# Performance work log

Hardware: AMD Instinct MI355X
Metric: run time of the kernel (lower is better)

The kernel has to match this reference:

```python
import jax, jax.numpy as jnp
from jax import lax
import numpy as np

# --- module constants (from init_kwargs) ---
MAXK = 512
BLOCK = 3            # Shi-Tomasi structure-tensor window
NUM_PAIRS = 256      # BAD descriptor dimensionality
ITERS = 20           # Sinkhorn iterations
EPS = 1.0            # entropy regularization
UNUSED = 1.0         # dustbin score
NMS_R = 3
THR = 0.0
PATCH_R = 8          # BAD pair-offset radius
BOX = 5              # BAD pre-smoothing box size

# fixed BAD comparison-pair offsets (dy1,dx1,dy2,dx2) -- constants, not learned
_OFFSETS = jnp.asarray(
    np.random.RandomState(42).randint(-PATCH_R, PATCH_R + 1, size=(NUM_PAIRS, 4)),
    dtype=jnp.int32)

_SOBEL_X = jnp.array([[-1., 0., 1.], [-2., 0., 2.], [-1., 0., 1.]], jnp.float32)[None, None]
_SOBEL_Y = jnp.transpose(_SOBEL_X, (0, 1, 3, 2))


def _conv(x, k):  # x: [B,1,H,W], k: [1,1,kh,kw]
    return lax.conv_general_dilated(x, k, (1, 1), 'SAME',
                                    dimension_numbers=('NCHW', 'OIHW', 'NCHW'))


def _detector(img):
    """Shi-Tomasi min-eigenvalue score map + dense BAD descriptor map."""
    Ix = _conv(img, _SOBEL_X)
    Iy = _conv(img, _SOBEL_Y)
    box = jnp.ones((1, 1, BLOCK, BLOCK), jnp.float32) / (BLOCK * BLOCK)
    Ixx = _conv(Ix * Ix, box)
    Iyy = _conv(Iy * Iy, box)
    Ixy = _conv(Ix * Iy, box)
    score = 0.5 * ((Ixx + Iyy) - jnp.sqrt((Ixx - Iyy) ** 2 + 4.0 * Ixy ** 2 + 1e-12))

    smooth = _conv(img, jnp.ones((1, 1, BOX, BOX), jnp.float32) / (BOX * BOX))[:, 0]  # [B,H,W]
    B, H, W = smooth.shape
    pad = jnp.pad(smooth, ((0, 0), (PATCH_R, PATCH_R), (PATCH_R, PATCH_R)), mode='edge')

    def one_pair(off):  # box-average difference at two shifted locations
        a = lax.dynamic_slice(pad, (0, PATCH_R + off[0], PATCH_R + off[1]), (B, H, W))
        b = lax.dynamic_slice(pad, (0, PATCH_R + off[2], PATCH_R + off[3]), (B, H, W))
        return a - b

    desc = jax.vmap(one_pair)(_OFFSETS)           # [D,B,H,W]
    return score[:, 0], jnp.transpose(desc, (1, 0, 2, 3))  # [B,H,W], [B,D,H,W]


def _nms_topk(score):
    """Max-pool NMS + top-k keypoint selection; invalid kpts = (-1,-1)."""
    win = 2 * NMS_R + 1
    mx = lax.reduce_window(score, -jnp.inf, lax.max, (1, win, win), (1, 1, 1), 'SAME')
    mask = (score >= mx) & (score > THR)
    B, H, W = score.shape
    masked = jnp.where(mask, score, -jnp.inf).reshape(B, H * W)
    vals, idx = lax.top_k(masked, MAXK)
    valid = jnp.isfinite(vals)
    y = (idx // W).astype(jnp.float32)
    x = (idx % W).astype(jnp.float32)
    kpts = jnp.where(valid[..., None], jnp.stack([y, x], -1), -1.0)  # [B,K,2] (y,x)
    return kpts


def _extract(desc_map, kpts):
    """Bilinear (subpixel) descriptor gather; zeros for invalid keypoints."""
    B, D, H, W = desc_map.shape
    valid = (kpts[:, :, 0] >= 0).astype(desc_map.dtype)
    y = jnp.clip(kpts[:, :, 0], 0.0, H - 1.0)
    x = jnp.clip(kpts[:, :, 1], 0.0, W - 1.0)
    y0 = jnp.floor(y); x0 = jnp.floor(x)
    y1 = jnp.minimum(y0 + 1.0, H - 1.0); x1 = jnp.minimum(x0 + 1.0, W - 1.0)
    wy = y - y0; wx = x - x0
    y0i, y1i = y0.astype(jnp.int32), y1.astype(jnp.int32)
    x0i, x1i = x0.astype(jnp.int32), x1.astype(jnp.int32)
    flat = desc_map.reshape(B, D, H * W)

    def g(yi, xi):  # [B,K] -> [B,D,K]
        return jnp.take_along_axis(flat, (yi * W + xi)[:, None, :], axis=2)

    d = (g(y0i, x0i) * ((1 - wy) * (1 - wx))[:, None, :]
         + g(y0i, x1i) * ((1 - wy) * wx)[:, None, :]
         + g(y1i, x0i) * (wy * (1 - wx))[:, None, :]
         + g(y1i, x1i) * (wy * wx)[:, None, :])
    return jnp.transpose(d, (0, 2, 1)) * valid[..., None]  # [B,K,D]


def _sinkhorn(d1, d2):
    """Log-domain Sinkhorn with dustbin row/col (SuperGlue-style OT)."""
    s1 = jnp.sum(d1 * d1, -1)
    s2 = jnp.sum(d2 * d2, -1)
    dist = jnp.sqrt(jnp.clip(
        s1[:, :, None] + s2[:, None, :] - 2.0 * jnp.einsum('bkd,bld->bkl', d1, d2),
        1e-12))
    B, K, _ = dist.shape
    Z = jnp.full((B, K + 1, K + 1), UNUSED / EPS, dtype=dist.dtype)
    Z = Z.at[:, :K, :K].set(-dist / EPS)
    norm = -jnp.log(2.0 * K)
    log_mu = jnp.concatenate([jnp.zeros((K,), Z.dtype),
                              jnp.log(jnp.full((1,), float(K), Z.dtype))]) + norm
    log_nu = log_mu

    def body(_, uv):
        u, v = uv
        u = log_mu - jax.scipy.special.logsumexp(Z + v[:, None, :], axis=2)
        v = log_nu - jax.scipy.special.logsumexp(Z + u[:, :, None], axis=1)
        return (u, v)

    u0 = jnp.zeros((B, K + 1), Z.dtype)
    u, v = lax.fori_loop(0, ITERS, body, (u0, u0))
    return jnp.exp(Z + u[:, :, None] + v[:, None, :] - norm)  # [B,K+1,K+1]


def _l2norm(d):
    return d / (jnp.linalg.norm(d, axis=-1, keepdims=True) + 1e-12)


def setup_inputs() -> dict:
    key = jax.random.key(0)
    k1, k2 = jax.random.split(key)
    image1 = jax.random.uniform(k1, (1, 1, 480, 640), jnp.float32)
    image2 = jax.random.uniform(k2, (1, 1, 480, 640), jnp.float32)
    return {"image1": image1, "image2": image2}


def reference(image1, image2):
    s1, m1 = _detector(image1)
    s2, m2 = _detector(image2)
    kpts1 = _nms_topk(s1)
    kpts2 = _nms_topk(s2)
    d1 = _l2norm(_extract(m1, kpts1))
    d2 = _l2norm(_extract(m2, kpts2))
    probs = _sinkhorn(d1, d2)
    return (kpts1, kpts2, probs)
```

## Files before the change

### kernel.cpp

```cpp
#include <hip/hip_runtime.h>
#include <math.h>
#include <stdint.h>

#define HH 480
#define WW 640
#define HW (HH*WW)
#define KK 512
#define DD 256
#define KP1 513
#define NSLOT 16
#define NBX 40
#define NBY 30
#define SLOTS_PER_IMG (NBX*NBY*NSLOT)
#define SVN 1024
#define SB 32
#define NORM_F (-6.9314718055994531f)
#define LOGK_F (6.2383246250395077f)
#define MU0 (1.0f/1024.0f)
#define MU1 (0.5f)

#define OFF_SURV   0u
#define OFF_Z      16384u
#define OFF_SMOOTH 2473984u
#define OFF_CAND   4931584u
#define OFF_KIDX   5238784u
#define OFF_DESC   5242880u
#define OFF_SBUF   6291456u
#define OFF_PCA    6295552u
#define OFF_PCB    6361216u
#define OFF_VA     6426880u
#define OFF_VB     6429184u
#define OFF_U      6431488u
#define OFF_SVCNT  6438912u

struct OffsTab { int v[1024]; };
static constexpr OffsTab make_offsets() {
  OffsTab o{};
  unsigned st[624] = {};
  st[0] = 42u;
  for (int i = 1; i < 624; ++i)
    st[i] = 1812433253u*(st[i-1] ^ (st[i-1] >> 30)) + (unsigned)i;
  int idx = 624, got = 0;
  while (got < 1024) {
    if (idx == 624) {
      for (int i = 0; i < 624; ++i) {
        unsigned y = (st[i] & 0x80000000u) | (st[(i+1)%624] & 0x7fffffffu);
        st[i] = st[(i+397)%624] ^ (y >> 1) ^ ((y & 1u) ? 2567483615u : 0u);
      }
      idx = 0;
    }
    unsigned y = st[idx++];
    y ^= y >> 11;
    y ^= (y << 7)  & 2636928640u;
    y ^= (y << 15) & 4022730752u;
    y ^= y >> 18;
    unsigned mv = y & 31u;
    if (mv <= 16u) { o.v[got] = (int)mv - 8; ++got; }
  }
  return o;
}
__device__ __constant__ OffsTab OFFS = make_offsets();

__global__ __launch_bounds__(256) void detnms_kernel(const float* __restrict__ img0,
    const float* __restrict__ img1, float* __restrict__ smooth,
    unsigned long long* __restrict__ cand) {
  __shared__ float tile[26][26];
  __shared__ float ixA[24][24], iyA[24][24];
  __shared__ float sc[22][22];
  __shared__ float vs[16][26];
  __shared__ float vm[16][22];
  __shared__ int wsum[4], wbase[4];
  const int imgI = blockIdx.z;
  const float* img = imgI ? img1 : img0;
  const int bx0 = blockIdx.x*16, by0 = blockIdx.y*16;
  const int tx = threadIdx.x, ty = threadIdx.y, lt = ty*16+tx;
  for (int p = lt; p < 676; p += 256) {
    int r = p/26, c = p%26;
    int gy = by0-5+r, gx = bx0-5+c;
    tile[r][c] = (gy >= 0 && gy < HH && gx >= 0 && gx < WW) ? img[gy*WW+gx] : 0.f;
  }
  __syncthreads();
  for (int p = lt; p < 576; p += 256) {
    int r = p/24, c = p%24;
    int gy = by0-4+r, gx = bx0-4+c;
    float ix = 0.f, iy = 0.f;
    if (gy >= 0 && gy < HH && gx >= 0 && gx < WW) {
      float t00 = tile[r][c],   t01 = tile[r][c+1],   t02 = tile[r][c+2];
      float t10 = tile[r+1][c],                        t12 = tile[r+1][c+2];
      float t20 = tile[r+2][c], t21 = tile[r+2][c+1], t22 = tile[r+2][c+2];
      ix = t00*(-1.f) + t02*1.f + t10*(-2.f) + t12*2.f + t20*(-1.f) + t22*1.f;
      iy = t00*(-1.f) + t01*(-2.f) + t02*(-1.f) + t20*1.f + t21*2.f + t22*1.f;
    }
    ixA[r][c] = ix; iyA[r][c] = iy;
  }
  __syncthreads();
  const float c9 = 1.f/9.f, c25 = 1.f/25.f;
  for (int p = lt; p < 484; p += 256) {
    int r = p/22, c = p%22;
    int gy = by0-3+r, gx = bx0-3+c;
    float v = -INFINITY;
    if (gy >= 0 && gy < HH && gx >= 0 && gx < WW) {
      float sxx = 0.f, syy = 0.f, sxy = 0.f;
      for (int dr = 0; dr < 3; ++dr)
        for (int dc = 0; dc < 3; ++dc) {
          float jx = ixA[r+dr][c+dc], jy = iyA[r+dr][c+dc];
          float pxxv = jx*jx, pyyv = jy*jy, pxyv = jx*jy;
          sxx += pxxv*c9; syy += pyyv*c9; sxy += pxyv*c9;
        }
      float tdif = sxx - syy;
      v = 0.5f * ((sxx + syy) - sqrtf(tdif*tdif + 4.f*(sxy*sxy) + 1e-12f));
    }
    sc[r][c] = v;
  }
  for (int p = lt; p < 416; p += 256) {
    int i = p/26, c = p%26;
    vs[i][c] = tile[i+3][c] + tile[i+4][c] + tile[i+5][c] + tile[i+6][c] + tile[i+7][c];
  }
  __syncthreads();
  for (int p = lt; p < 352; p += 256) {
    int i = p/22, c = p%22;
    float m = sc[i][c];
    m = fmaxf(m, sc[i+1][c]); m = fmaxf(m, sc[i+2][c]); m = fmaxf(m, sc[i+3][c]);
    m = fmaxf(m, sc[i+4][c]); m = fmaxf(m, sc[i+5][c]); m = fmaxf(m, sc[i+6][c]);
    vm[i][c] = m;
  }
  float sm = (vs[ty][tx+3] + vs[ty][tx+4] + vs[ty][tx+5] + vs[ty][tx+6] + vs[ty][tx+7]) * c25;
  smooth[imgI*HW + (by0+ty)*WW + (bx0+tx)] = sm;
  __syncthreads();
  float cv = sc[ty+3][tx+3];
  float m = vm[ty][tx];
  m = fmaxf(m, vm[ty][tx+1]); m = fmaxf(m, vm[ty][tx+2]); m = fmaxf(m, vm[ty][tx+3]);
  m = fmaxf(m, vm[ty][tx+4]); m = fmaxf(m, vm[ty][tx+5]); m = fmaxf(m, vm[ty][tx+6]);
  bool pred = (cv >= m && cv > 0.f);
  unsigned long long mask = __ballot(pred);
  int lane = lt & 63, wid = lt >> 6;
  if (lane == 0) wsum[wid] = __popcll(mask);
  __syncthreads();
  if (lt == 0) {
    int s0 = wsum[0], s1 = wsum[1], s2 = wsum[2], s3 = wsum[3];
    wbase[0] = 0; wbase[1] = s0; wbase[2] = s0+s1; wbase[3] = s0+s1+s2;
    wsum[0] = s0+s1+s2+s3;
  }
  __syncthreads();
  const int total = wsum[0];
  const size_t slotBase = (size_t)imgI*SLOTS_PER_IMG + (size_t)(blockIdx.y*NBX + blockIdx.x)*NSLOT;
  if (pred) {
    int pos = wbase[wid] + __popcll(mask & ((1ull << lane) - 1ull));
    if (pos < NSLOT) {
      int idx = (by0+ty)*WW + (bx0+tx);
      unsigned int ub = __float_as_uint(cv) | 0x80000000u;
      cand[slotBase + pos] = ((unsigned long long)ub << 32) | (unsigned int)(~idx);
    }
  }
  if (lt >= total && lt < NSLOT) cand[slotBase + lt] = 0ull;
}

__global__ __launch_bounds__(1024) void select2a_kernel(const unsigned long long* __restrict__ cand,
    unsigned long long* __restrict__ surv, int* __restrict__ svcnt) {
  __shared__ int hist[1024];
  __shared__ int sB1, sB2, sNeed, sCount;
  const int imgI = blockIdx.x, t = threadIdx.x;
  const unsigned long long* cd = cand + (size_t)imgI*SLOTS_PER_IMG;
  unsigned long long kreg[19];
  #pragma unroll
  for (int r = 0; r < 19; ++r) {
    int i = t + r*1024;
    kreg[r] = (i < SLOTS_PER_IMG) ? cd[i] : 0ull;
  }
  hist[t] = 0;
  if (t == 0) { sB1 = -1; sB2 = 0; sCount = 0; }
  __syncthreads();
  #pragma unroll
  for (int r = 0; r < 19; ++r)
    if (kreg[r]) atomicAdd(&hist[(int)(kreg[r] >> 54)], 1);
  __syncthreads();
  for (int d = 1; d < 1024; d <<= 1) {
    int vv = hist[t] + ((t + d < 1024) ? hist[t + d] : 0);
    __syncthreads();
    hist[t] = vv;
    __syncthreads();
  }
  if (hist[t] >= KK) atomicMax(&sB1, t);
  __syncthreads();
  const int b1 = sB1;
  if (t == 0 && b1 >= 0) sNeed = KK - ((b1 < 1023) ? hist[b1 + 1] : 0);
  __syncthreads();
  int b2 = 0;
  if (b1 >= 0) {
    hist[t] = 0;
    __syncthreads();
    #pragma unroll
    for (int r = 0; r < 19; ++r) {
      unsigned long long k = kreg[r];
      if (k && (int)(k >> 54) == b1) atomicAdd(&hist[(int)(k >> 44) & 1023], 1);
    }
    __syncthreads();
    for (int d = 1; d < 1024; d <<= 1) {
      int vv = hist[t] + ((t + d < 1024) ? hist[t + d] : 0);
      __syncthreads();
      hist[t] = vv;
      __syncthreads();
    }
    if (hist[t] >= sNeed) atomicMax(&sB2, t);
    __syncthreads();
    b2 = sB2;
  }
  #pragma unroll
  for (int r = 0; r < 19; ++r) {
    unsigned long long k = kreg[r];
    if (k) {
      int bin1 = (int)(k >> 54);
      if (bin1 > b1 || (bin1 == b1 && ((int)(k >> 44) & 1023) >= b2)) {
        int pos = atomicAdd(&sCount, 1);
        if (pos < SVN) surv[imgI*SVN + pos] = k;
      }
    }
  }
  __syncthreads();
  if (t == 0) svcnt[imgI] = (sCount < SVN) ? sCount : SVN;
}

__global__ __launch_bounds__(64) void rank_kernel(const unsigned long long* __restrict__ surv,
    const int* __restrict__ svcnt, float* __restrict__ kptsOut, int* __restrict__ kidx) {
  __shared__ unsigned long long sk[SVN];
  const int imgI = blockIdx.y, t = threadIdx.x;
  const int n = svcnt[imgI];
  for (int i = t; i < SVN; i += 64) sk[i] = (i < n) ? surv[imgI*SVN + i] : 0ull;
  __syncthreads();
  const int k = blockIdx.x*64 + t;
  if (k < n) {
    unsigned long long key = sk[k];
    int r = 0;
    for (int m = 0; m < n; ++m) r += (sk[m] > key) ? 1 : 0;
    if (r < KK) {
      int id = (int)(~(unsigned int)(key & 0xFFFFFFFFull));
      kptsOut[imgI*2*KK + 2*r]     = (float)(id / WW);
      kptsOut[imgI*2*KK + 2*r + 1] = (float)(id % WW);
      kidx[imgI*KK + r] = id;
    }
  } else if (k >= n && k < KK) {
    kptsOut[imgI*2*KK + 2*k]     = -1.f;
    kptsOut[imgI*2*KK + 2*k + 1] = -1.f;
    kidx[imgI*KK + k] = -1;
  }
}

__global__ __launch_bounds__(256) void desc_kernel(const float* __restrict__ smooth,
    const int* __restrict__ kidx, float* __restrict__ desc, float* __restrict__ sbuf) {
  __shared__ float wsum[4];
  const int k = blockIdx.x, imgI = blockIdx.y;
  const int j = threadIdx.x;
  const int id = kidx[imgI*KK + k];
  float val = 0.f;
  if (id >= 0) {
    int y = id / WW, x = id % WW;
    int o0 = OFFS.v[4*j], o1 = OFFS.v[4*j+1], o2 = OFFS.v[4*j+2], o3 = OFFS.v[4*j+3];
    const float* sm = smooth + imgI*HW;
    int ya = min(max(y+o0, 0), HH-1), xa = min(max(x+o1, 0), WW-1);
    int yb = min(max(y+o2, 0), HH-1), xb = min(max(x+o3, 0), WW-1);
    val = sm[ya*WW + xa] - sm[yb*WW + xb];
  }
  float ss = val*val;
  for (int off = 32; off; off >>= 1) ss += __shfl_down(ss, off);
  if ((j & 63) == 0) wsum[j >> 6] = ss;
  __syncthreads();
  if (j == 0) wsum[0] = wsum[0] + wsum[1] + wsum[2] + wsum[3];
  __syncthreads();
  float tot = wsum[0];
  float inv = 1.f / (sqrtf(tot) + 1e-12f);
  desc[((size_t)imgI*KK + k)*DD + j] = val * inv;
  if (j == 0) sbuf[imgI*KK + k] = tot * inv * inv;
}

__global__ __launch_bounds__(256) void zbuild_kernel(const float* __restrict__ desc,
    const float* __restrict__ sbuf, float* __restrict__ Z) {
  __shared__ float sA[16][260], sB[16][260];
  const int ty = threadIdx.y, tx = threadIdx.x;
  const int i0 = blockIdx.y*16, j0 = blockIdx.x*16;
  const int lt = ty*16 + tx;
  for (int p = lt; p < 16*DD; p += 256) {
    int r = p / DD, c = p % DD;
    sA[r][c] = desc[((size_t)0*KK + i0 + r)*DD + c];
    sB[r][c] = desc[((size_t)1*KK + j0 + r)*DD + c];
  }
  __syncthreads();
  const int i = i0 + ty, j = j0 + tx;
  const float4* pa = (const float4*)&sA[ty][0];
  const float4* pb = (const float4*)&sB[tx][0];
  float acc = 0.f;
  for (int c4 = 0; c4 < DD/4; ++c4) {
    float4 a = pa[c4], b = pb[c4];
    acc += a.x*b.x; acc += a.y*b.y; acc += a.z*b.z; acc += a.w*b.w;
  }
  float d2 = sbuf[0*KK + i] + sbuf[KK + j] - 2.f*acc;
  Z[(size_t)i*KK + j] = -sqrtf(fmaxf(d2, 1e-12f));
}

__global__ __launch_bounds__(1024) void sink_step_kernel(const float* __restrict__ Z,
    const float* __restrict__ PcolIn, float* __restrict__ PcolOut,
    const float* __restrict__ vIn, float* __restrict__ vOut,
    float* __restrict__ uBuf, float* __restrict__ probs, int mode) {
  __shared__ float v[KP1];
  __shared__ float pcolw[16][KP1];
  const int t = threadIdx.x, b = blockIdx.x;
  const int widx = t >> 6, lane = t & 63;
  const int gw = b*16 + widx;
  if (mode == 0) {
    for (int j = t; j < KP1; j += 1024) v[j] = 0.f;
  } else {
    for (int j = t; j < KP1; j += 1024) {
      float s = 0.f;
      #pragma unroll
      for (int w = 0; w < SB; ++w) s += PcolIn[w*KP1 + j];
      float lognu = (j < KK) ? NORM_F : (LOGK_F + NORM_F);
      v[j] = lognu + vIn[j] - logf(s);
    }
  }
  __syncthreads();
  const int j0 = lane*8;
  const float4 va = *(const float4*)&v[j0];
  const float4 vb = *(const float4*)&v[j0+4];
  const float vv[8] = {va.x, va.y, va.z, va.w, vb.x, vb.y, vb.z, vb.w};
  const int nrows = (gw == 511) ? 2 : 1;
  if (mode == 2) {
    for (int rr = 0; rr < nrows; ++rr) {
      const int r = rr ? 512 : gw;
      float* pr = probs + (size_t)r*KP1;
      const float ur = uBuf[r];
      float zv[8];
      if (r < 512) {
        float4 z0 = *(const float4*)&Z[(size_t)r*KK + j0];
        float4 z1 = *(const float4*)&Z[(size_t)r*KK + j0 + 4];
        zv[0]=z0.x; zv[1]=z0.y; zv[2]=z0.z; zv[3]=z0.w;
        zv[4]=z1.x; zv[5]=z1.y; zv[6]=z1.z; zv[7]=z1.w;
      } else {
        #pragma unroll
        for (int q = 0; q < 8; ++q) zv[q] = 1.0f;
      }
      #pragma unroll
      for (int q = 0; q < 8; ++q) pr[j0+q] = expf(zv[q] + ur + vv[q] - NORM_F);
      if (lane == 0) pr[512] = expf(1.0f + ur + v[512] - NORM_F);
    }
    return;
  }
  float pacc[8]; float pacc8 = 0.f;
  #pragma unroll
  for (int q = 0; q < 8; ++q) pacc[q] = 0.f;
  for (int rr = 0; rr < nrows; ++rr) {
    const int r = rr ? 512 : gw;
    float zv[8];
    if (r < 512) {
      float4 z0 = *(const float4*)&Z[(size_t)r*KK + j0];
      float4 z1 = *(const float4*)&Z[(size_t)r*KK + j0 + 4];
      zv[0]=z0.x; zv[1]=z0.y; zv[2]=z0.z; zv[3]=z0.w;
      zv[4]=z1.x; zv[5]=z1.y; zv[6]=z1.z; zv[7]=z1.w;
    } else {
      #pragma unroll
      for (int q = 0; q < 8; ++q) zv[q] = 1.0f;
    }
    float tv[8]; float S = 0.f;
    #pragma unroll
    for (int q = 0; q < 8; ++q) { tv[q] = expf(zv[q] + vv[q]); S += tv[q]; }
    float t8 = 0.f;
    if (lane == 0) { t8 = expf(1.0f + v[512]); S += t8; }
    #pragma unroll
    for (int off = 32; off; off >>= 1) S += __shfl_xor(S, off);
    float mu = (r < 512) ? MU0 : MU1;
    float eu = mu / S;
    if (lane == 0) uBuf[r] = logf(eu);
    #pragma unroll
    for (int q = 0; q < 8; ++q) pacc[q] += tv[q] * eu;
    pacc8 += t8 * eu;
  }
  #pragma unroll
  for (int q = 0; q < 8; ++q) pcolw[widx][j0+q] = pacc[q];
  if (lane == 0) pcolw[widx][512] = pacc8;
  __syncthreads();
  float* pc = PcolOut + (size_t)b*KP1;
  for (int j = t; j < KP1; j += 1024) {
    float s = 0.f;
    #pragma unroll
    for (int w = 0; w < 16; ++w) s += pcolw[w][j];
    pc[j] = s;
  }
  if (b == 0) {
    for (int j = t; j < KP1; j += 1024) vOut[j] = v[j];
  }
}

extern "C" void kernel_launch(void* const* d_in, const int* in_sizes, int n_in,
                              void* d_out, int out_size, void* d_ws, size_t ws_size,
                              hipStream_t stream) {
  const float* img1 = (const float*)d_in[0];
  const float* img2 = (const float*)d_in[1];
  float* out = (float*)d_out;
  char* ws = (char*)d_ws;

  unsigned long long* surv = (unsigned long long*)(ws + OFF_SURV);
  float* smooth = (float*)(ws + OFF_SMOOTH);
  unsigned long long* cand = (unsigned long long*)(ws + OFF_CAND);
  int*   kidx   = (int*)  (ws + OFF_KIDX);
  float* desc   = (float*)(ws + OFF_DESC);
  float* sbuf   = (float*)(ws + OFF_SBUF);
  float* Z      = (float*)(ws + OFF_Z);
  float* pcA    = (float*)(ws + OFF_PCA);
  float* pcB    = (float*)(ws + OFF_PCB);
  float* vA     = (float*)(ws + OFF_VA);
  float* vB     = (float*)(ws + OFF_VB);
  float* uBuf   = (float*)(ws + OFF_U);
  int*   svcnt  = (int*)  (ws + OFF_SVCNT);
  float* probsOut = out + 2*KK*2;

  detnms_kernel<<<dim3(NBX, NBY, 2), dim3(16, 16), 0, stream>>>(img1, img2, smooth, cand);
  select2a_kernel<<<2, 1024, 0, stream>>>(cand, surv, svcnt);
  rank_kernel<<<dim3(16, 2), 64, 0, stream>>>(surv, svcnt, out, kidx);
  desc_kernel<<<dim3(KK, 2), 256, 0, stream>>>(smooth, kidx, desc, sbuf);
  zbuild_kernel<<<dim3(32, 32), dim3(16, 16), 0, stream>>>(desc, sbuf, Z);

  sink_step_kernel<<<SB, 1024, 0, stream>>>(Z, pcB, pcA, vB, vA, uBuf, probsOut, 0);
  int ping = 0;
  for (int it = 1; it < 20; ++it) {
    float* pin  = ping ? pcB : pcA;
    float* pout = ping ? pcA : pcB;
    float* vin  = ping ? vB  : vA;
    float* vout = ping ? vA  : vB;
    sink_step_kernel<<<SB, 1024, 0, stream>>>(Z, pin, pout, vin, vout, uBuf, probsOut, 1);
    ping ^= 1;
  }
  {
    float* pin = ping ? pcB : pcA;
    float* vin = ping ? vB  : vA;
    sink_step_kernel<<<SB, 1024, 0, stream>>>(Z, pin, pcA, vin, vA, uBuf, probsOut, 2);
  }
}
```

Before: 162.8 us.

## Fuse Sinkhorn iterations into one cooperative kernel with grid flag barriers

Replaces the 21 per-iteration Sinkhorn launches with a single cooperative kernel of 32 blocks. The blocks sync through release/acquire flag barriers in global memory, and v stays in shared memory across iterations. Also merges rank into the select kernel so the survivor round-trip through global memory goes away, and makes zbuild compute a 2x2 register tile per thread. This removes launch overhead and kernel boundaries, at the cost of spin-wait barriers plus an extra memset and a cooperative launch.

```diff
diff --git a/kernel.cpp b/kernel.cpp
--- a/kernel.cpp
+++ b/kernel.cpp
@@ -12,26 +12,21 @@
 #define NBX 40
 #define NBY 30
 #define SLOTS_PER_IMG (NBX*NBY*NSLOT)
-#define SVN 1024
+#define SVCAP 2048
 #define SB 32
 #define NORM_F (-6.9314718055994531f)
 #define LOGK_F (6.2383246250395077f)
 #define MU0 (1.0f/1024.0f)
 #define MU1 (0.5f)
 
-#define OFF_SURV   0u
+#define OFF_FLAGS  0u
 #define OFF_Z      16384u
 #define OFF_SMOOTH 2473984u
 #define OFF_CAND   4931584u
 #define OFF_KIDX   5238784u
 #define OFF_DESC   5242880u
 #define OFF_SBUF   6291456u
-#define OFF_PCA    6295552u
-#define OFF_PCB    6361216u
-#define OFF_VA     6426880u
-#define OFF_VB     6429184u
-#define OFF_U      6431488u
-#define OFF_SVCNT  6438912u
+#define OFF_PC     6295552u
 
 struct OffsTab { int v[1024]; };
 static constexpr OffsTab make_offsets() {
@@ -155,8 +150,9 @@
   if (lt >= total && lt < NSLOT) cand[slotBase + lt] = 0ull;
 }
 
-__global__ __launch_bounds__(1024) void select2a_kernel(const unsigned long long* __restrict__ cand,
-    unsigned long long* __restrict__ surv, int* __restrict__ svcnt) {
+__global__ __launch_bounds__(1024) void select2_kernel(const unsigned long long* __restrict__ cand,
+    float* __restrict__ kptsOut, int* __restrict__ kidx) {
+  __shared__ unsigned long long sk[SVCAP];
   __shared__ int hist[1024];
   __shared__ int sB1, sB2, sNeed, sCount;
   const int imgI = blockIdx.x, t = threadIdx.x;
@@ -212,24 +208,19 @@
       int bin1 = (int)(k >> 54);
       if (bin1 > b1 || (bin1 == b1 && ((int)(k >> 44) & 1023) >= b2)) {
         int pos = atomicAdd(&sCount, 1);
-        if (pos < SVN) surv[imgI*SVN + pos] = k;
+        if (pos < SVCAP) sk[pos] = k;
       }
     }
   }
   __syncthreads();
-  if (t == 0) svcnt[imgI] = (sCount < SVN) ? sCount : SVN;
-}
-
-__global__ __launch_bounds__(64) void rank_kernel(const unsigned long long* __restrict__ surv,
-    const int* __restrict__ svcnt, float* __restrict__ kptsOut, int* __restrict__ kidx) {
-  __shared__ unsigned long long sk[SVN];
-  const int imgI = blockIdx.y, t = threadIdx.x;
-  const int n = svcnt[imgI];
-  for (int i = t; i < SVN; i += 64) sk[i] = (i < n) ? surv[imgI*SVN + i] : 0ull;
-  __syncthreads();
-  const int k = blockIdx.x*64 + t;
-  if (k < n) {
-    unsigned long long key = sk[k];
+  const int n = (sCount < SVCAP) ? sCount : SVCAP;
+  for (int k = n + t; k < KK; k += 1024) {
+    kptsOut[imgI*2*KK + 2*k]     = -1.f;
+    kptsOut[imgI*2*KK + 2*k + 1] = -1.f;
+    kidx[imgI*KK + k] = -1;
+  }
+  for (int i = t; i < n; i += 1024) {
+    unsigned long long key = sk[i];
     int r = 0;
     for (int m = 0; m < n; ++m) r += (sk[m] > key) ? 1 : 0;
     if (r < KK) {
@@ -238,10 +229,6 @@
       kptsOut[imgI*2*KK + 2*r + 1] = (float)(id % WW);
       kidx[imgI*KK + r] = id;
     }
-  } else if (k >= n && k < KK) {
-    kptsOut[imgI*2*KK + 2*k]     = -1.f;
-    kptsOut[imgI*2*KK + 2*k + 1] = -1.f;
-    kidx[imgI*KK + k] = -1;
   }
 }
 
@@ -274,90 +261,67 @@
 
 __global__ __launch_bounds__(256) void zbuild_kernel(const float* __restrict__ desc,
     const float* __restrict__ sbuf, float* __restrict__ Z) {
-  __shared__ float sA[16][260], sB[16][260];
+  __shared__ float sA[32][260], sB[32][260];
   const int ty = threadIdx.y, tx = threadIdx.x;
-  const int i0 = blockIdx.y*16, j0 = blockIdx.x*16;
+  const int i0 = blockIdx.y*32, j0 = blockIdx.x*32;
   const int lt = ty*16 + tx;
-  for (int p = lt; p < 16*DD; p += 256) {
-    int r = p / DD, c = p % DD;
-    sA[r][c] = desc[((size_t)0*KK + i0 + r)*DD + c];
-    sB[r][c] = desc[((size_t)1*KK + j0 + r)*DD + c];
-  }
-  __syncthreads();
-  const int i = i0 + ty, j = j0 + tx;
-  const float4* pa = (const float4*)&sA[ty][0];
-  const float4* pb = (const float4*)&sB[tx][0];
-  float acc = 0.f;
+  for (int p = lt; p < 32*DD; p += 256) {
+    int r = p >> 8, c = p & 255;
+    sA[r][c] = desc[((size_t)(i0 + r))*DD + c];
+    sB[r][c] = desc[((size_t)(KK + j0 + r))*DD + c];
+  }
+  __syncthreads();
+  const float4* pa0 = (const float4*)&sA[ty][0];
+  const float4* pa1 = (const float4*)&sA[ty+16][0];
+  const float4* pb0 = (const float4*)&sB[tx][0];
+  const float4* pb1 = (const float4*)&sB[tx+16][0];
+  float a00 = 0.f, a01 = 0.f, a10 = 0.f, a11 = 0.f;
   for (int c4 = 0; c4 < DD/4; ++c4) {
-    float4 a = pa[c4], b = pb[c4];
-    acc += a.x*b.x; acc += a.y*b.y; acc += a.z*b.z; acc += a.w*b.w;
-  }
-  float d2 = sbuf[0*KK + i] + sbuf[KK + j] - 2.f*acc;
-  Z[(size_t)i*KK + j] = -sqrtf(fmaxf(d2, 1e-12f));
-}
-
-__global__ __launch_bounds__(1024) void sink_step_kernel(const float* __restrict__ Z,
-    const float* __restrict__ PcolIn, float* __restrict__ PcolOut,
-    const float* __restrict__ vIn, float* __restrict__ vOut,
-    float* __restrict__ uBuf, float* __restrict__ probs, int mode) {
+    float4 a0 = pa0[c4], a1 = pa1[c4], b0 = pb0[c4], b1 = pb1[c4];
+    a00 += a0.x*b0.x; a00 += a0.y*b0.y; a00 += a0.z*b0.z; a00 += a0.w*b0.w;
+    a01 += a0.x*b1.x; a01 += a0.y*b1.y; a01 += a0.z*b1.z; a01 += a0.w*b1.w;
+    a10 += a1.x*b0.x; a10 += a1.y*b0.y; a10 += a1.z*b0.z; a10 += a1.w*b0.w;
+    a11 += a1.x*b1.x; a11 += a1.y*b1.y; a11 += a1.z*b1.z; a11 += a1.w*b1.w;
+  }
+  const float s0 = sbuf[i0 + ty], s0b = sbuf[i0 + ty + 16];
+  const float s1 = sbuf[KK + j0 + tx], s1b = sbuf[KK + j0 + tx + 16];
+  Z[(size_t)(i0+ty)   *KK + j0+tx]    = -sqrtf(fmaxf(s0  + s1  - 2.f*a00, 1e-12f));
+  Z[(size_t)(i0+ty)   *KK + j0+tx+16] = -sqrtf(fmaxf(s0  + s1b - 2.f*a01, 1e-12f));
+  Z[(size_t)(i0+ty+16)*KK + j0+tx]    = -sqrtf(fmaxf(s0b + s1  - 2.f*a10, 1e-12f));
+  Z[(size_t)(i0+ty+16)*KK + j0+tx+16] = -sqrtf(fmaxf(s0b + s1b - 2.f*a11, 1e-12f));
+}
+
+__global__ __launch_bounds__(1024) void sinkhorn_kernel(const float* __restrict__ Z,
+    float* __restrict__ Pcol, int* flags, float* __restrict__ probs) {
   __shared__ float v[KP1];
-  __shared__ float pcolw[16][KP1];
+  __shared__ float pcolw[16][516];
   const int t = threadIdx.x, b = blockIdx.x;
   const int widx = t >> 6, lane = t & 63;
   const int gw = b*16 + widx;
-  if (mode == 0) {
-    for (int j = t; j < KP1; j += 1024) v[j] = 0.f;
-  } else {
-    for (int j = t; j < KP1; j += 1024) {
-      float s = 0.f;
-      #pragma unroll
-      for (int w = 0; w < SB; ++w) s += PcolIn[w*KP1 + j];
-      float lognu = (j < KK) ? NORM_F : (LOGK_F + NORM_F);
-      v[j] = lognu + vIn[j] - logf(s);
-    }
-  }
-  __syncthreads();
   const int j0 = lane*8;
-  const float4 va = *(const float4*)&v[j0];
-  const float4 vb = *(const float4*)&v[j0+4];
-  const float vv[8] = {va.x, va.y, va.z, va.w, vb.x, vb.y, vb.z, vb.w};
-  const int nrows = (gw == 511) ? 2 : 1;
-  if (mode == 2) {
-    for (int rr = 0; rr < nrows; ++rr) {
-      const int r = rr ? 512 : gw;
-      float* pr = probs + (size_t)r*KP1;
-      const float ur = uBuf[r];
-      float zv[8];
-      if (r < 512) {
-        float4 z0 = *(const float4*)&Z[(size_t)r*KK + j0];
-        float4 z1 = *(const float4*)&Z[(size_t)r*KK + j0 + 4];
-        zv[0]=z0.x; zv[1]=z0.y; zv[2]=z0.z; zv[3]=z0.w;
-        zv[4]=z1.x; zv[5]=z1.y; zv[6]=z1.z; zv[7]=z1.w;
-      } else {
+  const bool hasDust = (gw == 511);
+  for (int j = t; j < KP1; j += 1024) v[j] = 0.f;
+  __syncthreads();
+  float uMain = 0.f, uDust = 0.f;
+  for (int it = 0; it < 20; ++it) {
+    if (it > 0) {
+      const float* pcAll = Pcol + ((it-1)&1)*(SB*KP1);
+      for (int j = t; j < KP1; j += 1024) {
+        float s = 0.f;
         #pragma unroll
-        for (int q = 0; q < 8; ++q) zv[q] = 1.0f;
+        for (int w = 0; w < SB; ++w) s += pcAll[w*KP1 + j];
+        float lognu = (j < KK) ? NORM_F : (LOGK_F + NORM_F);
+        v[j] = lognu + v[j] - logf(s);
       }
-      #pragma unroll
-      for (int q = 0; q < 8; ++q) pr[j0+q] = expf(zv[q] + ur + vv[q] - NORM_F);
-      if (lane == 0) pr[512] = expf(1.0f + ur + v[512] - NORM_F);
-    }
-    return;
-  }
-  float pacc[8]; float pacc8 = 0.f;
-  #pragma unroll
-  for (int q = 0; q < 8; ++q) pacc[q] = 0.f;
-  for (int rr = 0; rr < nrows; ++rr) {
-    const int r = rr ? 512 : gw;
-    float zv[8];
-    if (r < 512) {
-      float4 z0 = *(const float4*)&Z[(size_t)r*KK + j0];
-      float4 z1 = *(const float4*)&Z[(size_t)r*KK + j0 + 4];
-      zv[0]=z0.x; zv[1]=z0.y; zv[2]=z0.z; zv[3]=z0.w;
-      zv[4]=z1.x; zv[5]=z1.y; zv[6]=z1.z; zv[7]=z1.w;
-    } else {
-      #pragma unroll
-      for (int q = 0; q < 8; ++q) zv[q] = 1.0f;
-    }
+      __syncthreads();
+    }
+    float4 va = *(const float4*)&v[j0];
+    float4 vb = *(const float4*)&v[j0+4];
+    float vv[8] = {va.x,va.y,va.z,va.w,vb.x,vb.y,vb.z,vb.w};
+    const float* zr = Z + (size_t)gw*KK;
+    float4 z0 = *(const float4*)&zr[j0];
+    float4 z1 = *(const float4*)&zr[j0+4];
+    float zv[8] = {z0.x,z0.y,z0.z,z0.w,z1.x,z1.y,z1.z,z1.w};
     float tv[8]; float S = 0.f;
     #pragma unroll
     for (int q = 0; q < 8; ++q) { tv[q] = expf(zv[q] + vv[q]); S += tv[q]; }
@@ -365,26 +329,85 @@
     if (lane == 0) { t8 = expf(1.0f + v[512]); S += t8; }
     #pragma unroll
     for (int off = 32; off; off >>= 1) S += __shfl_xor(S, off);
-    float mu = (r < 512) ? MU0 : MU1;
-    float eu = mu / S;
-    if (lane == 0) uBuf[r] = logf(eu);
+    float eu = MU0 / S;
+    uMain = logf(eu);
+    float pacc[8]; float pacc8 = t8 * eu;
     #pragma unroll
-    for (int q = 0; q < 8; ++q) pacc[q] += tv[q] * eu;
-    pacc8 += t8 * eu;
-  }
+    for (int q = 0; q < 8; ++q) pacc[q] = tv[q] * eu;
+    if (hasDust) {
+      float tv2[8]; float S2 = 0.f;
+      #pragma unroll
+      for (int q = 0; q < 8; ++q) { tv2[q] = expf(1.0f + vv[q]); S2 += tv2[q]; }
+      float t82 = 0.f;
+      if (lane == 0) { t82 = expf(1.0f + v[512]); S2 += t82; }
+      #pragma unroll
+      for (int off = 32; off; off >>= 1) S2 += __shfl_xor(S2, off);
+      float eu2 = MU1 / S2;
+      uDust = logf(eu2);
+      #pragma unroll
+      for (int q = 0; q < 8; ++q) pacc[q] += tv2[q] * eu2;
+      pacc8 += t82 * eu2;
+    }
+    *(float4*)&pcolw[widx][j0]   = make_float4(pacc[0], pacc[1], pacc[2], pacc[3]);
+    *(float4*)&pcolw[widx][j0+4] = make_float4(pacc[4], pacc[5], pacc[6], pacc[7]);
+    if (lane == 0) pcolw[widx][512] = pacc8;
+    __syncthreads();
+    float* pc = Pcol + (it&1)*(SB*KP1) + b*KP1;
+    for (int j = t; j < KP1; j += 1024) {
+      float s = 0.f;
+      #pragma unroll
+      for (int w = 0; w < 16; ++w) s += pcolw[w][j];
+      pc[j] = s;
+    }
+    __syncthreads();
+    const int gen = it + 1;
+    if (t == 0)
+      __hip_atomic_store(&flags[b], gen, __ATOMIC_RELEASE, __HIP_MEMORY_SCOPE_AGENT);
+    if (t < SB) {
+      int spins = 0;
+      while (__hip_atomic_load(&flags[t], __ATOMIC_RELAXED, __HIP_MEMORY_SCOPE_AGENT) < gen) {
+        __builtin_amdgcn_s_sleep(2);
+        if (++spins == 1024) {
+          while (__hip_atomic_load(&flags[t], __ATOMIC_ACQUIRE, __HIP_MEMORY_SCOPE_AGENT) < gen)
+            __builtin_amdgcn_s_sleep(8);
+          break;
+        }
+      }
+    }
+    __syncthreads();
+    if (t == 0) {
+      if (__hip_atomic_load(&flags[b], __ATOMIC_ACQUIRE, __HIP_MEMORY_SCOPE_AGENT) < 0)
+        flags[b] = 0;
+    }
+    __syncthreads();
+  }
+  {
+    const float* pcAll = Pcol + ((19)&1)*(SB*KP1);
+    for (int j = t; j < KP1; j += 1024) {
+      float s = 0.f;
+      #pragma unroll
+      for (int w = 0; w < SB; ++w) s += pcAll[w*KP1 + j];
+      float lognu = (j < KK) ? NORM_F : (LOGK_F + NORM_F);
+      v[j] = lognu + v[j] - logf(s);
+    }
+    __syncthreads();
+  }
+  float4 va = *(const float4*)&v[j0];
+  float4 vb = *(const float4*)&v[j0+4];
+  float vv[8] = {va.x,va.y,va.z,va.w,vb.x,vb.y,vb.z,vb.w};
+  const float* zr = Z + (size_t)gw*KK;
+  float4 z0 = *(const float4*)&zr[j0];
+  float4 z1 = *(const float4*)&zr[j0+4];
+  float zv[8] = {z0.x,z0.y,z0.z,z0.w,z1.x,z1.y,z1.z,z1.w};
+  float* pr = probs + (size_t)gw*KP1;
   #pragma unroll
-  for (int q = 0; q < 8; ++q) pcolw[widx][j0+q] = pacc[q];
-  if (lane == 0) pcolw[widx][512] = pacc8;
-  __syncthreads();
-  float* pc = PcolOut + (size_t)b*KP1;
-  for (int j = t; j < KP1; j += 1024) {
-    float s = 0.f;
+  for (int q = 0; q < 8; ++q) pr[j0+q] = expf(zv[q] + uMain + vv[q] - NORM_F);
+  if (lane == 0) pr[512] = expf(1.0f + uMain + v[512] - NORM_F);
+  if (hasDust) {
+    float* pd = probs + (size_t)512*KP1;
     #pragma unroll
-    for (int w = 0; w < 16; ++w) s += pcolw[w][j];
-    pc[j] = s;
-  }
-  if (b == 0) {
-    for (int j = t; j < KP1; j += 1024) vOut[j] = v[j];
+    for (int q = 0; q < 8; ++q) pd[j0+q] = expf(1.0f + uDust + vv[q] - NORM_F);
+    if (lane == 0) pd[512] = expf(1.0f + uDust + v[512] - NORM_F);
   }
 }
 
@@ -396,40 +419,24 @@
   float* out = (float*)d_out;
   char* ws = (char*)d_ws;
 
-  unsigned long long* surv = (unsigned long long*)(ws + OFF_SURV);
+  int*   flags  = (int*)  (ws + OFF_FLAGS);
   float* smooth = (float*)(ws + OFF_SMOOTH);
   unsigned long long* cand = (unsigned long long*)(ws + OFF_CAND);
   int*   kidx   = (int*)  (ws + OFF_KIDX);
   float* desc   = (float*)(ws + OFF_DESC);
   float* sbuf   = (float*)(ws + OFF_SBUF);
   float* Z      = (float*)(ws + OFF_Z);
-  float* pcA    = (float*)(ws + OFF_PCA);
-  float* pcB    = (float*)(ws + OFF_PCB);
-  float* vA     = (float*)(ws + OFF_VA);
-  float* vB     = (float*)(ws + OFF_VB);
-  float* uBuf   = (float*)(ws + OFF_U);
-  int*   svcnt  = (int*)  (ws + OFF_SVCNT);
+  float* pcol   = (float*)(ws + OFF_PC);
   float* probsOut = out + 2*KK*2;
 
+  hipMemsetAsync(ws + OFF_FLAGS, 0, 128, stream);
+
   detnms_kernel<<<dim3(NBX, NBY, 2), dim3(16, 16), 0, stream>>>(img1, img2, smooth, cand);
-  select2a_kernel<<<2, 1024, 0, stream>>>(cand, surv, svcnt);
-  rank_kernel<<<dim3(16, 2), 64, 0, stream>>>(surv, svcnt, out, kidx);
+  select2_kernel<<<2, 1024, 0, stream>>>(cand, out, kidx);
   desc_kernel<<<dim3(KK, 2), 256, 0, stream>>>(smooth, kidx, desc, sbuf);
-  zbuild_kernel<<<dim3(32, 32), dim3(16, 16), 0, stream>>>(desc, sbuf, Z);
-
-  sink_step_kernel<<<SB, 1024, 0, stream>>>(Z, pcB, pcA, vB, vA, uBuf, probsOut, 0);
-  int ping = 0;
-  for (int it = 1; it < 20; ++it) {
-    float* pin  = ping ? pcB : pcA;
-    float* pout = ping ? pcA : pcB;
-    float* vin  = ping ? vB  : vA;
-    float* vout = ping ? vA  : vB;
-    sink_step_kernel<<<SB, 1024, 0, stream>>>(Z, pin, pout, vin, vout, uBuf, probsOut, 1);
-    ping ^= 1;
-  }
-  {
-    float* pin = ping ? pcB : pcA;
-    float* vin = ping ? vB  : vA;
-    sink_step_kernel<<<SB, 1024, 0, stream>>>(Z, pin, pcA, vin, vA, uBuf, probsOut, 2);
-  }
-}
+  zbuild_kernel<<<dim3(16, 16), dim3(16, 16), 0, stream>>>(desc, sbuf, Z);
+
+  void* args[] = { (void*)&Z, (void*)&pcol, (void*)&flags, (void*)&probsOut };
+  hipLaunchCooperativeKernel((const void*)sinkhorn_kernel, dim3(SB), dim3(1024),
+                             args, 0, stream);
+}
```

Measured after the change: 195.0 us. 1.2x slower.
